# Kernel optimization log

Measured on AMD Instinct MI355X. Metric: run time of the kernel, lower is better.

## Reference

```python
import math
import jax, jax.numpy as jnp
import numpy as np

B, T, C, H = 2, 2048, 1024, 16
HD = C // H
ALPHA = 32.0


def setup_inputs() -> dict:
    key = jax.random.key(0)
    ks = jax.random.split(key, 16)
    s = 0.02
    inp = {
        "query": jax.random.normal(ks[0], (B, T, C), jnp.float32),
        "key": jax.random.normal(ks[1], (B, T, C), jnp.float32),
        "value": jax.random.normal(ks[2], (B, T, C), jnp.float32),
        # causal mask: 0 => masked (matches masked_fill(att_mask == 0, -inf))
        "att_mask": jnp.tril(jnp.ones((1, 1, T, T), jnp.float32)),
        "Wq": jax.random.normal(ks[3], (C, C), jnp.float32) * s,
        "bq": jnp.zeros((C,), jnp.float32),
        "Wk": jax.random.normal(ks[4], (C, C), jnp.float32) * s,
        "bk": jnp.zeros((C,), jnp.float32),
        "Wv": jax.random.normal(ks[5], (C, C), jnp.float32) * s,
        "bv": jnp.zeros((C,), jnp.float32),
        "Wp": jax.random.normal(ks[6], (C, C), jnp.float32) * s,
        "bp": jnp.zeros((C,), jnp.float32),
    }
    return inp


def reference(query, key, value, att_mask, Wq, bq, Wk, bk, Wv, bv, Wp, bp):
    b, tq, c = query.shape
    tk = key.shape[1]
    # separate QKV projections, split heads: [B,H,T,HD]
    q = (query @ Wq + bq).reshape(b, tq, H, HD).transpose(0, 2, 1, 3)
    k = (key @ Wk + bk).reshape(b, tk, H, HD).transpose(0, 2, 1, 3)
    v = (value @ Wv + bv).reshape(b, tk, H, HD).transpose(0, 2, 1, 3)
    # PBrelax: pre-scale q by 1/(alpha*sqrt(hd)), subtract detached global abs-max, rescale
    att = jnp.einsum("bhqd,bhkd->bhqk", q * (1.0 / ALPHA / math.sqrt(HD)), k)
    att = (att - jax.lax.stop_gradient(jnp.max(jnp.abs(att)))) * ALPHA
    att = jnp.where(att_mask[:, :, :tq, :tk] == 0, -jnp.inf, att)
    att = jax.nn.softmax(att, axis=-1)
    y = jnp.einsum("bhqk,bhkd->bhqd", att, v)
    y = y.transpose(0, 2, 1, 3).reshape(b, tq, c)
    return y @ Wp + bp
```

## Files before the change

kernel.cpp:

```cpp
#include <hip/hip_runtime.h>


#define Bsz 2
#define Tsz 2048
#define Csz 1024
#define Hsz 16
#define HDsz 64

typedef __bf16 bf16;
typedef __bf16 bf16x8 __attribute__((ext_vector_type(8)));
typedef __bf16 bf16x4 __attribute__((ext_vector_type(4)));
typedef float float4v __attribute__((ext_vector_type(4)));

#define MFMA16(a, b, c) __builtin_amdgcn_mfma_f32_16x16x32_bf16(a, b, c, 0, 0, 0)

#define GLOAD_LDS16(gptr, lptr)                                      \
  __builtin_amdgcn_global_load_lds(                                  \
      (const __attribute__((address_space(1))) void*)(gptr),         \
      (__attribute__((address_space(3))) void*)(lptr), 16, 0, 0)

__global__ __launch_bounds__(256) void prep_bf16(
    const float* __restrict__ q, const float* __restrict__ k,
    const float* __restrict__ v, bf16* __restrict__ oq,
    bf16* __restrict__ ok, bf16* __restrict__ ov,
    const float* __restrict__ Wq, const float* __restrict__ Wk,
    const float* __restrict__ Wv, const float* __restrict__ Wp,
    bf16* __restrict__ WT) {
  __shared__ float Ts[64][68];
  const int bid = (int)blockIdx.x;
  const int tid = threadIdx.x;
  if (bid < 6144) {
    const int z = bid >> 11;
    const int xb = bid & 2047;
    const float* src = z == 0 ? q : (z == 1 ? k : v);
    bf16* dst = z == 0 ? oq : (z == 1 ? ok : ov);
    const size_t i = ((size_t)xb * 256 + tid) * 8;
    const float4 a = *(const float4*)(src + i);
    const float4 b = *(const float4*)(src + i + 4);
    bf16x8 o;
    o[0] = (bf16)a.x; o[1] = (bf16)a.y; o[2] = (bf16)a.z; o[3] = (bf16)a.w;
    o[4] = (bf16)b.x; o[5] = (bf16)b.y; o[6] = (bf16)b.z; o[7] = (bf16)b.w;
    *(bf16x8*)(dst + i) = o;
  } else {
    const int w = bid - 6144;
    const int z = w >> 8;
    const int rem = w & 255;
    const int k0 = (rem >> 4) * 64, n0 = (rem & 15) * 64;
    const float* W = z == 0 ? Wq : (z == 1 ? Wk : (z == 2 ? Wv : Wp));
    bf16* out = WT + (size_t)z * (Csz * Csz);
#pragma unroll
    for (int it = 0; it < 4; ++it) {
      const int idx = it * 256 + tid;
      const int r = idx >> 4, c4 = (idx & 15) * 4;
      *(float4*)&Ts[r][c4] =
          *(const float4*)(W + (size_t)(k0 + r) * Csz + n0 + c4);
    }
    __syncthreads();
#pragma unroll
    for (int it = 0; it < 2; ++it) {
      const int idx = it * 256 + tid;
      const int n = idx & 63, k8 = (idx >> 6) * 8;
      bf16x8 o;
#pragma unroll
      for (int j = 0; j < 8; ++j) o[j] = (bf16)Ts[k8 + j][n];
      *(bf16x8*)(out + (size_t)(n0 + n) * Csz + k0 + k8) = o;
    }
  }
}

__global__ __launch_bounds__(1024, 4) void gemm256_qkv(
    const bf16* __restrict__ A0, const bf16* __restrict__ A1,
    const bf16* __restrict__ A2, const bf16* __restrict__ Wt,
    const float* __restrict__ b0, const float* __restrict__ b1,
    const float* __restrict__ b2, bf16* __restrict__ C0,
    bf16* __restrict__ C1, bf16* __restrict__ Vt) {
  constexpr int NT = Csz / 64;
  const int z = blockIdx.z;
  const bf16* A = z == 0 ? A0 : (z == 1 ? A1 : A2);
  const float* bias = z == 0 ? b0 : (z == 1 ? b1 : b2);
  const bf16* Bt = Wt + (size_t)z * (Csz * Csz);
  const int m0 = blockIdx.y * 256;
  const int nz0 = blockIdx.x * 256;

  __shared__ bf16 As[2 * 256 * 64];
  __shared__ bf16 Bs[2 * 256 * 64];

  const int tid = threadIdx.x;
  const int wave = tid >> 6, lane = tid & 63;
  const int l15 = lane & 15, quad = lane >> 4;
  const int wm = wave >> 2, wn = wave & 3;

  const int srow = tid >> 3;
  const int sch = tid & 7;
  const bf16* Ab = A + (size_t)(m0 + srow) * Csz + (sch ^ (srow & 7)) * 8;
  const bf16* Bb = Bt + (size_t)(nz0 + srow) * Csz + (sch ^ (srow & 7)) * 8;

#define STAGE(lbuf, tt)                                                      \
  {                                                                          \
    GLOAD_LDS16(Ab + (size_t)(tt)*64, &As[(lbuf) * (256 * 64) + tid * 8]);   \
    GLOAD_LDS16(Ab + (size_t)128 * Csz + (size_t)(tt)*64,                    \
                &As[(lbuf) * (256 * 64) + 8192 + tid * 8]);                  \
    GLOAD_LDS16(Bb + (size_t)(tt)*64, &Bs[(lbuf) * (256 * 64) + tid * 8]);   \
    GLOAD_LDS16(Bb + (size_t)128 * Csz + (size_t)(tt)*64,                    \
                &Bs[(lbuf) * (256 * 64) + 8192 + tid * 8]);                  \
  }
#define RD_A(dst, lbuf, i2, ks)                                              \
  dst = *(const bf16x8*)&As[(lbuf) * (256 * 64) +                            \
                            (wm * 64 + (i2)*16 + l15) * 64 +                 \
                            ((((ks)*4 + quad) ^ (l15 & 7)) * 8)];
#define RD_B(dst, lbuf, j2, ks)                                              \
  dst = *(const bf16x8*)&Bs[(lbuf) * (256 * 64) +                            \
                            (wn * 64 + (j2)*16 + l15) * 64 +                 \
                            ((((ks)*4 + quad) ^ (l15 & 7)) * 8)];

  float4v acc[4][4];
#pragma unroll
  for (int i = 0; i < 4; ++i)
#pragma unroll
    for (int j = 0; j < 4; ++j) acc[i][j] = (float4v){0.f, 0.f, 0.f, 0.f};

  STAGE(0, 0);
  asm volatile("s_waitcnt vmcnt(0)" ::: "memory");
  __builtin_amdgcn_s_barrier();
  __builtin_amdgcn_sched_barrier(0);

#pragma unroll 1
  for (int t = 0; t < NT; ++t) {
    const int buf = t & 1;
    if (t + 1 < NT) STAGE(buf ^ 1, t + 1);

    bf16x8 af[4][2], bfr[4][2];
#pragma unroll
    for (int i = 0; i < 4; ++i) {
      RD_A(af[i][0], buf, i, 0);
      RD_A(af[i][1], buf, i, 1);
    }
#pragma unroll
    for (int j = 0; j < 4; ++j) {
      RD_B(bfr[j][0], buf, j, 0);
      RD_B(bfr[j][1], buf, j, 1);
    }
#pragma unroll
    for (int i = 0; i < 4; ++i)
#pragma unroll
      for (int j = 0; j < 4; ++j) {
        acc[i][j] = MFMA16(af[i][0], bfr[j][0], acc[i][j]);
        acc[i][j] = MFMA16(af[i][1], bfr[j][1], acc[i][j]);
      }

    if (t + 1 < NT) {
      asm volatile("s_waitcnt vmcnt(0)" ::: "memory");
    }
    __builtin_amdgcn_sched_barrier(0);
    __builtin_amdgcn_s_barrier();
    __builtin_amdgcn_sched_barrier(0);
  }
#undef STAGE
#undef RD_A
#undef RD_B

  const int omb0 = m0 + wm * 64 + quad * 4;
  const int onb0 = nz0 + wn * 64 + l15;
  if (z == 2) {
#pragma unroll
    for (int j = 0; j < 4; ++j) {
      const int n = onb0 + j * 16;
      const float bj = bias[n];
#pragma unroll
      for (int i = 0; i < 4; ++i) {
        const int mrow = omb0 + i * 16;
        const int bb = mrow >> 11, tt = mrow & (Tsz - 1);
        union { bf16 h[4]; uint2 u; } pk;
#pragma unroll
        for (int r = 0; r < 4; ++r) pk.h[r] = (bf16)(acc[i][j][r] + bj);
        *(uint2*)(Vt + ((size_t)(bb * 1024 + n)) * Tsz + tt) = pk.u;
      }
    }
  } else {
    bf16* C = z == 0 ? C0 : C1;
    const float osc = z == 0 ? 0.180336880111124f : 1.0f;
#pragma unroll
    for (int j = 0; j < 4; ++j) {
      const float bj = bias[onb0 + j * 16];
#pragma unroll
      for (int i = 0; i < 4; ++i) {
#pragma unroll
        for (int r = 0; r < 4; ++r) {
          const float v = (acc[i][j][r] + bj) * osc;
          C[(size_t)(omb0 + i * 16 + r) * Csz + onb0 + j * 16] = (bf16)v;
        }
      }
    }
  }
}

__global__ __launch_bounds__(256) void gemm_op(
    const bf16* __restrict__ A, const bf16* __restrict__ Bt,
    const float* __restrict__ bias, float* __restrict__ C) {
  __shared__ bf16 As[128 * 32];
  __shared__ bf16 Bs[64 * 32];
  const int tid = threadIdx.x;
  const int wave = tid >> 6, lane = tid & 63;
  const int l15 = lane & 15, quad = lane >> 4;
  const int m0 = blockIdx.y * 128, n0 = blockIdx.x * 64;
  const int wm = (wave >> 1) * 64, wn = (wave & 1) * 32;
  const int srow = tid >> 2, schunk = tid & 3;

  float4v acc[4][2];
#pragma unroll
  for (int i = 0; i < 4; ++i)
#pragma unroll
    for (int j = 0; j < 2; ++j) acc[i][j] = (float4v){0.f, 0.f, 0.f, 0.f};

  for (int k0 = 0; k0 < Csz; k0 += 32) {
    __syncthreads();
#pragma unroll
    for (int p = 0; p < 2; ++p) {
      const int row = p * 64 + srow;
      GLOAD_LDS16(A + (size_t)(m0 + row) * Csz + k0 + schunk * 8,
                  &As[(p * 256 + tid) * 8]);
    }
    GLOAD_LDS16(Bt + (size_t)(n0 + srow) * Csz + k0 + schunk * 8,
                &Bs[tid * 8]);
    __syncthreads();

    bf16x8 af[4], bfr[2];
#pragma unroll
    for (int i = 0; i < 4; ++i)
      af[i] = *(const bf16x8*)&As[(wm + i * 16 + l15) * 32 + quad * 8];
#pragma unroll
    for (int j = 0; j < 2; ++j)
      bfr[j] = *(const bf16x8*)&Bs[(wn + j * 16 + l15) * 32 + quad * 8];
#pragma unroll
    for (int i = 0; i < 4; ++i)
#pragma unroll
      for (int j = 0; j < 2; ++j)
        acc[i][j] = MFMA16(af[i], bfr[j], acc[i][j]);
  }

  const int omb = m0 + wm + quad * 4;
  const int onb = n0 + wn + l15;
#pragma unroll
  for (int j = 0; j < 2; ++j) {
    const float bj = bias[onb + j * 16];
#pragma unroll
    for (int i = 0; i < 4; ++i) {
#pragma unroll
      for (int r = 0; r < 4; ++r)
        C[(size_t)(omb + i * 16 + r) * Csz + onb + j * 16] =
            acc[i][j][r] + bj;
    }
  }
}

__global__ __launch_bounds__(512) void attn_mfma(const bf16* __restrict__ Q,
                                                 const bf16* __restrict__ K,
                                                 const bf16* __restrict__ Vt,
                                                 bf16* __restrict__ Y) {
  __shared__ bf16 Ks[2][64 * 64];
  __shared__ bf16 Vs[2][64 * 64];
  __shared__ bf16 Ps[8][16 * 72];

  const int bh = blockIdx.y;
  const int b = bh >> 4, h = bh & 15;
  int xr = (blockIdx.x & 1) ? (int)(gridDim.x - 1 - (blockIdx.x >> 1))
                            : (int)(blockIdx.x >> 1);
  if (bh >= 16) xr = (int)(gridDim.x - 1) - xr;
  const int i0 = xr * 128;
  const int tid = threadIdx.x;
  const int wave = tid >> 6, lane = tid & 63;
  const int l15 = lane & 15, quad = lane >> 4;

  const int srow = tid >> 3;
  const int sch = tid & 7;

  const bf16* kb = K + (size_t)b * Tsz * Csz + h * HDsz;
  const bf16* vb = Vt + (size_t)bh * HDsz * Tsz;

  const int qb = i0 + wave * 16;

  bf16x8 qf[2];
  {
    const bf16* qp =
        Q + ((size_t)(b * Tsz + qb + l15)) * Csz + h * HDsz + quad * 8;
    qf[0] = *(const bf16x8*)qp;
    qf[1] = *(const bf16x8*)(qp + 32);
  }

  bf16x8 ones;
#pragma unroll
  for (int j = 0; j < 8; ++j) ones[j] = (bf16)1.0f;

  float4v Of[4];
  float4v accl = (float4v){0.f, 0.f, 0.f, 0.f};
#pragma unroll
  for (int nc = 0; nc < 4; ++nc) Of[nc] = (float4v){0.f, 0.f, 0.f, 0.f};

  const int ntile = i0 / 64 + 2;

#define STAGE_KV(tt, bb)                                                     \
  {                                                                          \
    const int c = sch ^ (srow & 7);                                          \
    GLOAD_LDS16(kb + (size_t)((tt)*64 + srow) * Csz + c * 8,                 \
                &Ks[bb][tid * 8]);                                           \
    GLOAD_LDS16(vb + (size_t)srow * Tsz + (tt)*64 + c * 8,                   \
                &Vs[bb][tid * 8]);                                           \
  }

  STAGE_KV(0, 0);
  asm volatile("s_waitcnt vmcnt(0)" ::: "memory");
  __builtin_amdgcn_s_barrier();
  __builtin_amdgcn_sched_barrier(0);

#pragma unroll 1
  for (int t = 0; t < ntile; ++t) {
    const int j0 = t * 64;
    const int buf = t & 1;
    if (t + 1 < ntile) STAGE_KV(t + 1, buf ^ 1);

    if (j0 <= qb + 15) {
      float4v S[4];
#pragma unroll
      for (int nc = 0; nc < 4; ++nc) {
        const int row = nc * 16 + l15;
        const bf16x8 k0 =
            *(const bf16x8*)&Ks[buf][row * 64 + ((quad ^ (row & 7)) * 8)];
        const bf16x8 k1 =
            *(const bf16x8*)&Ks[buf][row * 64 + (((quad + 4) ^ (row & 7)) * 8)];
        float4v a = (float4v){0.f, 0.f, 0.f, 0.f};
        a = MFMA16(k0, qf[0], a);
        a = MFMA16(k1, qf[1], a);
        S[nc] = a;
      }

      if (j0 + 63 > qb) {
        const int q = qb + l15;
#pragma unroll
        for (int nc = 0; nc < 4; ++nc) {
          const int keyb = j0 + nc * 16 + quad * 4;
#pragma unroll
          for (int r = 0; r < 4; ++r)
            if (keyb + r > q) S[nc][r] = -1e30f;
        }
      }

#pragma unroll
      for (int nc = 0; nc < 4; ++nc) {
        bf16x4 pk;
#pragma unroll
        for (int r = 0; r < 4; ++r)
          pk[r] = (bf16)__builtin_amdgcn_exp2f(S[nc][r]);
        *(bf16x4*)&Ps[wave][l15 * 72 + nc * 16 + quad * 4] = pk;
      }

      bf16x8 pf[2];
#pragma unroll
      for (int kc = 0; kc < 2; ++kc)
        pf[kc] = *(const bf16x8*)&Ps[wave][l15 * 72 + kc * 32 + quad * 8];
      accl = MFMA16(ones, pf[0], accl);
      accl = MFMA16(ones, pf[1], accl);
#pragma unroll
      for (int nc = 0; nc < 4; ++nc) {
        const int row = nc * 16 + l15;
#pragma unroll
        for (int kc = 0; kc < 2; ++kc) {
          const bf16x8 vf = *(const bf16x8*)
              &Vs[buf][row * 64 + (((kc * 4 + quad) ^ (row & 7)) * 8)];
          Of[nc] = MFMA16(vf, pf[kc], Of[nc]);
        }
      }
    }

    if (t + 1 < ntile) {
      asm volatile("s_waitcnt vmcnt(0)" ::: "memory");
    }
    __builtin_amdgcn_sched_barrier(0);
    __builtin_amdgcn_s_barrier();
    __builtin_amdgcn_sched_barrier(0);
  }
#undef STAGE_KV

  {
    const float rl = __builtin_amdgcn_rcpf(accl[0]);
    const size_t rowoff = ((size_t)(b * Tsz + qb + l15)) * Csz + h * HDsz;
#pragma unroll
    for (int nc = 0; nc < 4; ++nc) {
      union { bf16 h4[4]; uint2 u; } pk;
#pragma unroll
      for (int r = 0; r < 4; ++r) pk.h4[r] = (bf16)(Of[nc][r] * rl);
      *(uint2*)(Y + rowoff + nc * 16 + quad * 4) = pk.u;
    }
  }
}

extern "C" void kernel_launch(void* const* d_in, const int* in_sizes, int n_in,
                              void* d_out, int out_size, void* d_ws,
                              size_t ws_size, hipStream_t stream) {
  const float* query = (const float*)d_in[0];
  const float* key = (const float*)d_in[1];
  const float* value = (const float*)d_in[2];
  const float* Wq = (const float*)d_in[4];
  const float* bq = (const float*)d_in[5];
  const float* Wk = (const float*)d_in[6];
  const float* bk = (const float*)d_in[7];
  const float* Wv = (const float*)d_in[8];
  const float* bv = (const float*)d_in[9];
  const float* Wp = (const float*)d_in[10];
  const float* bp = (const float*)d_in[11];
  float* out = (float*)d_out;

  char* ws = (char*)d_ws;
  bf16* WT = (bf16*)(ws);
  bf16* vc = (bf16*)(ws + (8u << 20));
  bf16* Qp = (bf16*)(ws + (16u << 20));
  bf16* Kp = (bf16*)(ws + (24u << 20));
  bf16* Vt = (bf16*)(ws + (32u << 20));
  bf16* Yb = vc;
  bf16* qc = (bf16*)d_out;
  bf16* kc = (bf16*)((char*)d_out + (8u << 20));

  const int M = Bsz * Tsz;

  prep_bf16<<<dim3(7168), dim3(256), 0, stream>>>(query, key, value, qc, kc,
                                                  vc, Wq, Wk, Wv, Wp, WT);
  gemm256_qkv<<<dim3(Csz / 256, M / 256, 3), dim3(1024), 0, stream>>>(
      qc, kc, vc, WT, bq, bk, bv, Qp, Kp, Vt);
  attn_mfma<<<dim3(Tsz / 128, Bsz * Hsz), dim3(512), 0, stream>>>(Qp, Kp, Vt,
                                                                  Yb);
  gemm_op<<<dim3(Csz / 64, M / 128), dim3(256), 0, stream>>>(
      Yb, WT + 3u * (Csz * Csz), bp, out);
}
```

Measured before the change: 228.9 us.

## Triple-buffer A tiles in QKV GEMM to prefetch two stages ahead

```diff
diff --git a/kernel.cpp b/kernel.cpp
--- a/kernel.cpp
+++ b/kernel.cpp
@@ -82,7 +82,7 @@
   const int m0 = blockIdx.y * 256;
   const int nz0 = blockIdx.x * 256;
 
-  __shared__ bf16 As[2 * 256 * 64];
+  __shared__ bf16 As[3 * 256 * 64];
   __shared__ bf16 Bs[2 * 256 * 64];
 
   const int tid = threadIdx.x;
@@ -95,11 +95,14 @@
   const bf16* Ab = A + (size_t)(m0 + srow) * Csz + (sch ^ (srow & 7)) * 8;
   const bf16* Bb = Bt + (size_t)(nz0 + srow) * Csz + (sch ^ (srow & 7)) * 8;
 
-#define STAGE(lbuf, tt)                                                      \
+#define STAGE_A(lbuf, tt)                                                    \
   {                                                                          \
     GLOAD_LDS16(Ab + (size_t)(tt)*64, &As[(lbuf) * (256 * 64) + tid * 8]);   \
     GLOAD_LDS16(Ab + (size_t)128 * Csz + (size_t)(tt)*64,                    \
                 &As[(lbuf) * (256 * 64) + 8192 + tid * 8]);                  \
+  }
+#define STAGE_B(lbuf, tt)                                                    \
+  {                                                                          \
     GLOAD_LDS16(Bb + (size_t)(tt)*64, &Bs[(lbuf) * (256 * 64) + tid * 8]);   \
     GLOAD_LDS16(Bb + (size_t)128 * Csz + (size_t)(tt)*64,                    \
                 &Bs[(lbuf) * (256 * 64) + 8192 + tid * 8]);                  \
@@ -119,26 +122,31 @@
 #pragma unroll
     for (int j = 0; j < 4; ++j) acc[i][j] = (float4v){0.f, 0.f, 0.f, 0.f};
 
-  STAGE(0, 0);
-  asm volatile("s_waitcnt vmcnt(0)" ::: "memory");
+  STAGE_A(0, 0);
+  STAGE_B(0, 0);
+  STAGE_A(1, 1);
+  asm volatile("s_waitcnt vmcnt(2)" ::: "memory");
   __builtin_amdgcn_s_barrier();
   __builtin_amdgcn_sched_barrier(0);
 
+  int abuf = 0;
 #pragma unroll 1
   for (int t = 0; t < NT; ++t) {
-    const int buf = t & 1;
-    if (t + 1 < NT) STAGE(buf ^ 1, t + 1);
+    const int bbuf = t & 1;
+    const int ast = abuf == 0 ? 2 : abuf - 1;
+    if (t + 1 < NT) STAGE_B(bbuf ^ 1, t + 1);
+    if (t + 2 < NT) STAGE_A(ast, t + 2);
 
     bf16x8 af[4][2], bfr[4][2];
 #pragma unroll
     for (int i = 0; i < 4; ++i) {
-      RD_A(af[i][0], buf, i, 0);
-      RD_A(af[i][1], buf, i, 1);
+      RD_A(af[i][0], abuf, i, 0);
+      RD_A(af[i][1], abuf, i, 1);
     }
 #pragma unroll
     for (int j = 0; j < 4; ++j) {
-      RD_B(bfr[j][0], buf, j, 0);
-      RD_B(bfr[j][1], buf, j, 1);
+      RD_B(bfr[j][0], bbuf, j, 0);
+      RD_B(bfr[j][1], bbuf, j, 1);
     }
 #pragma unroll
     for (int i = 0; i < 4; ++i)
@@ -148,14 +156,18 @@
         acc[i][j] = MFMA16(af[i][1], bfr[j][1], acc[i][j]);
       }
 
-    if (t + 1 < NT) {
+    if (t + 2 < NT) {
+      asm volatile("s_waitcnt vmcnt(2)" ::: "memory");
+    } else if (t + 1 < NT) {
       asm volatile("s_waitcnt vmcnt(0)" ::: "memory");
     }
     __builtin_amdgcn_sched_barrier(0);
     __builtin_amdgcn_s_barrier();
     __builtin_amdgcn_sched_barrier(0);
-  }
-#undef STAGE
+    abuf = abuf == 2 ? 0 : abuf + 1;
+  }
+#undef STAGE_A
+#undef STAGE_B
 #undef RD_A
 #undef RD_B
 
```

Result: no change. 229.9 us (+0.4%).
